# Kernel optimization log

Hardware: AMD Instinct MI355X
Metric: run time of the kernel (lower is better)

Reference implementation:

```python
import jax, jax.numpy as jnp
import numpy as np

B, C, H, W = 2, 64, 96, 96
HEADS, POOL, RED = 4, 2, 16
DH = C // HEADS  # dim_head = 16


def _conv1x1(x, Wt, b):
    # 1x1 conv == channelwise linear: Wt [Cout, Cin], x [B,Cin,H,W]
    return jnp.einsum('oc,bchw->bohw', Wt, x) + b[None, :, None, None]


def setup_inputs() -> dict:
    key = jax.random.key(0)
    ks = jax.random.split(key, 16)
    def w(k, shape, fan):
        return (jax.random.normal(k, shape, jnp.float32) / np.sqrt(fan)).astype(jnp.float32)
    x = jax.random.normal(ks[0], (B, C, H, W), jnp.float32)
    return {
        'x': x,
        'Wq': w(ks[1], (C, C), C), 'bq': jnp.zeros((C,), jnp.float32),
        'Wk': w(ks[2], (C, C), C), 'bk': jnp.zeros((C,), jnp.float32),
        'Wv': w(ks[3], (C, C), C), 'bv': jnp.zeros((C,), jnp.float32),
        'Wo': w(ks[4], (C, C), C), 'bo': jnp.zeros((C,), jnp.float32),
        'W1': w(ks[5], (C // RED, C), C), 'b1': jnp.zeros((C // RED,), jnp.float32),
        'W2': w(ks[6], (C, C // RED), C // RED), 'b2': jnp.zeros((C,), jnp.float32),
        'Wg': w(ks[7], (C, 2 * C), 2 * C), 'bg': jnp.zeros((C,), jnp.float32),
    }


def reference(x, Wq, bq, Wk, bk, Wv, bv, Wo, bo, W1, b1, W2, b2, Wg, bg):
    b, c, h, wdt = x.shape
    # --- MHSA with KV avg-pool downsampling (use_zoom=False -> zoomed_x = x) ---
    q = _conv1x1(x, Wq, bq)
    k = _conv1x1(x, Wk, bk)
    v = _conv1x1(x, Wv, bv)
    kh_, kw_ = h // POOL, wdt // POOL
    k = k.reshape(b, c, kh_, POOL, kw_, POOL).mean(axis=(3, 5))  # AvgPool2d(POOL)
    v = v.reshape(b, c, kh_, POOL, kw_, POOL).mean(axis=(3, 5))
    # reshape to heads: [B, heads, N, dh]
    qh = q.reshape(b, HEADS, DH, h * wdt).transpose(0, 1, 3, 2)
    kh = k.reshape(b, HEADS, DH, kh_ * kw_).transpose(0, 1, 3, 2)
    vh = v.reshape(b, HEADS, DH, kh_ * kw_).transpose(0, 1, 3, 2)
    scale = 1.0 / np.sqrt(DH)
    attn = jax.nn.softmax(jnp.einsum('bhqd,bhkd->bhqk', qh, kh) * scale, axis=-1)
    out = jnp.einsum('bhqk,bhkd->bhqd', attn, vh)  # [B,heads,N,dh]
    out = out.transpose(0, 1, 3, 2).reshape(b, c, h, wdt)
    attn_out = _conv1x1(out, Wo, bo)
    # --- SE excitation ---
    gap = attn_out.mean(axis=(2, 3))                      # [B,C]
    se = jax.nn.relu(gap @ W1.T + b1)                     # [B,C/r]
    ca = jax.nn.sigmoid(se @ W2.T + b2)                   # [B,C]
    enhanced = attn_out * ca[:, :, None, None]
    # --- residual fusion (use_zoom=False path) ---
    fused = x + enhanced
    # --- learned gate: concat GAPs -> 1x1 conv -> sigmoid -> blend ---
    gi = jnp.concatenate([x.mean(axis=(2, 3)), fused.mean(axis=(2, 3))], axis=1)  # [B,2C]
    gate = jax.nn.sigmoid(gi @ Wg.T + bg)[:, :, None, None]                       # [B,C,1,1]
    return x * (1.0 - gate) + fused * gate
```

## Files before the change

### kernel.cpp

```cpp
#include <hip/hip_runtime.h>
#include <hip/hip_bf16.h>

#define NPIX 9216
#define MKEY 2304

typedef __bf16 bf16x8 __attribute__((ext_vector_type(8)));
typedef float f32x4 __attribute__((ext_vector_type(4)));
typedef float f32x16 __attribute__((ext_vector_type(16)));
typedef short short8v __attribute__((ext_vector_type(8)));
typedef unsigned int u32x4v __attribute__((ext_vector_type(4)));

static __device__ __forceinline__ short f2bs(float f) {
  __bf16 h = (__bf16)f;
  return __builtin_bit_cast(short, h);
}

static __device__ __forceinline__ short4 pack4(const f32x16& acc, int q0, float4 bv, float scl) {
  short4 s;
  s.x = f2bs((acc[q0 + 0] + bv.x) * scl);
  s.y = f2bs((acc[q0 + 1] + bv.y) * scl);
  s.z = f2bs((acc[q0 + 2] + bv.z) * scl);
  s.w = f2bs((acc[q0 + 3] + bv.w) * scl);
  return s;
}

static __device__ __forceinline__ bf16x8 ldf8(const float* p) {
  float4 a = *(const float4*)p;
  float4 b = *(const float4*)(p + 4);
  bf16x8 f;
  f[0] = (__bf16)a.x; f[1] = (__bf16)a.y; f[2] = (__bf16)a.z; f[3] = (__bf16)a.w;
  f[4] = (__bf16)b.x; f[5] = (__bf16)b.y; f[6] = (__bf16)b.z; f[7] = (__bf16)b.w;
  return f;
}

__global__ __launch_bounds__(256) void proj_kernel(const float* __restrict__ x,
                                                   const float* __restrict__ Wq,
                                                   const float* __restrict__ bq,
                                                   const float* __restrict__ Wk,
                                                   const float* __restrict__ bk,
                                                   const float* __restrict__ Wv,
                                                   const float* __restrict__ bv,
                                                   short* __restrict__ qout,
                                                   short* __restrict__ kout,
                                                   short* __restrict__ vout,
                                                   short* __restrict__ onesb,
                                                   float* __restrict__ mxpart) {
  __shared__ float xs[64 * 128];
  int jid = blockIdx.x;
  int t = threadIdx.x;
  int w = t >> 6, lane = t & 63;
  int c31 = lane & 31, h5 = lane >> 5;
  bool isQ = jid < 144;
  int b, n0;
  if (isQ) { b = jid / 72; n0 = (jid % 72) * 128; }
  else { int j2 = jid - 144; b = j2 / 18; n0 = (j2 % 18) * 128; }

  if (jid == 0 && t < 160) {
    short8v ov;
#pragma unroll
    for (int j = 0; j < 8; j++) ov[j] = (short)0x3F80;
    *(short8v*)(onesb + t * 8) = ov;
  }

  if (isQ) {
#pragma unroll
    for (int i = 0; i < 8; i++) {
      int idx4 = t + 256 * i;
      int ci = idx4 >> 5, px4 = idx4 & 31;
      float4 v = *(const float4*)(x + ((size_t)(b * 64 + ci)) * NPIX + n0 + px4 * 4);
      *(float4*)(xs + ci * 128 + px4 * 4) = v;
    }
  } else {
#pragma unroll
    for (int it = 0; it < 32; it++) {
      int idx = t + 256 * it;
      int ci = idx >> 7, pm = idx & 127;
      int m = n0 + pm;
      int i = m / 48, j = m - i * 48;
      const float* s = x + ((size_t)(b * 64 + ci)) * NPIX + (2 * i) * 96 + 2 * j;
      float2 a = *(const float2*)(s);
      float2 c = *(const float2*)(s + 96);
      xs[ci * 128 + pm] = 0.25f * (a.x + a.y + c.x + c.y);
    }
  }
  __syncthreads();

  int px = w * 32 + c31;
  bf16x8 xf[4];
#pragma unroll
  for (int ks = 0; ks < 4; ks++) {
    bf16x8 f;
#pragma unroll
    for (int j = 0; j < 8; j++) f[j] = (__bf16)xs[(ks * 16 + h5 * 8 + j) * 128 + px];
    xf[ks] = f;
  }

  if (isQ) {
    int ci = t >> 2, qq = t & 3;
    const float* row = xs + ci * 128 + qq * 32;
    float s = 0.f;
#pragma unroll
    for (int i = 0; i < 32; i++) s += row[i];
    s += __shfl_xor(s, 1, 64);
    s += __shfl_xor(s, 2, 64);
    if (qq == 0) mxpart[jid * 64 + ci] = s;
  }
  __syncthreads();

  short* sv = (short*)xs;
  const float QSCALE = 0.25f * 1.44269504088896f;
  int nsets = isQ ? 1 : 2;

  for (int set = 0; set < nsets; set++) {
    const float* W = isQ ? Wq : (set ? Wv : Wk);
    const float* bias = isQ ? bq : (set ? bv : bk);
#pragma unroll
    for (int oc = 0; oc < 2; oc++) {
      bf16x8 wf[4];
#pragma unroll
      for (int ks = 0; ks < 4; ks++)
        wf[ks] = ldf8(W + (size_t)(oc * 32 + c31) * 64 + ks * 16 + h5 * 8);
      f32x16 acc = {};
#pragma unroll
      for (int ks = 0; ks < 4; ks++)
        acc = __builtin_amdgcn_mfma_f32_32x32x16_bf16(wf[ks], xf[ks], acc, 0, 0, 0);

      const float* bb = bias + oc * 32 + 4 * h5;
      float4 bv0 = *(const float4*)(bb);
      float4 bv1 = *(const float4*)(bb + 8);
      float4 bv2 = *(const float4*)(bb + 16);
      float4 bv3 = *(const float4*)(bb + 24);

      if (isQ || set == 0) {
        short* outp = isQ ? qout : kout;
        size_t NP = isQ ? NPIX : MKEY;
        float scl = isQ ? QSCALE : 1.0f;
        short* p0 = outp + (((size_t)(b * 4 + oc * 2)) * NP + n0 + px) * 16;
        short* p1 = outp + (((size_t)(b * 4 + oc * 2 + 1)) * NP + n0 + px) * 16;
        *(short4*)(p0 + 4 * h5) = pack4(acc, 0, bv0, scl);
        *(short4*)(p0 + 8 + 4 * h5) = pack4(acc, 4, bv1, scl);
        *(short4*)(p1 + 4 * h5) = pack4(acc, 8, bv2, scl);
        *(short4*)(p1 + 8 + 4 * h5) = pack4(acc, 12, bv3, scl);
      } else {
        float4 bvs[4] = {bv0, bv1, bv2, bv3};
#pragma unroll
        for (int g = 0; g < 4; g++) {
          int rowb = oc * 32 + 8 * g + 4 * h5;
          const float4& bv = bvs[g];
          sv[(rowb + 0) * 128 + px] = f2bs(acc[g * 4 + 0] + bv.x);
          sv[(rowb + 1) * 128 + px] = f2bs(acc[g * 4 + 1] + bv.y);
          sv[(rowb + 2) * 128 + px] = f2bs(acc[g * 4 + 2] + bv.z);
          sv[(rowb + 3) * 128 + px] = f2bs(acc[g * 4 + 3] + bv.w);
        }
      }
    }
  }

  if (!isQ) {
    __syncthreads();
#pragma unroll
    for (int kx = 0; kx < 4; kx++) {
      int idx8 = t + 256 * kx;
      int co = idx8 >> 4, pm8 = idx8 & 15;
      short8v v = *(short8v*)(sv + co * 128 + pm8 * 8);
      *(short8v*)(vout + ((size_t)(b * 64 + co)) * MKEY + n0 + pm8 * 8) = v;
    }
  }
}

__global__ __launch_bounds__(256, 3) void attn_kernel(const short* __restrict__ qb,
                                                      const short* __restrict__ kb,
                                                      const short* __restrict__ vb,
                                                      const short* __restrict__ onesb,
                                                      short* __restrict__ aob,
                                                      float* __restrict__ papart) {
  __shared__ __align__(16) float xch[3][3][64 * 12];
  int tid = threadIdx.x;
  int w = tid >> 6, lane = tid & 63;
  int c31 = lane & 31, h5 = lane >> 5;
  int h = blockIdx.y, b = blockIdx.z;
  int bh = b * 4 + h;
  int q0 = blockIdx.x * 96;

  bf16x8 qf[3];
#pragma unroll
  for (int qt = 0; qt < 3; qt++)
    qf[qt] = *(const bf16x8*)(qb + ((size_t)bh * NPIX + q0 + qt * 32 + c31) * 16 + h5 * 8);

  const short* kBh = kb + ((size_t)bh * MKEY + w * 576) * 16;
  const short* vsrc = (c31 < 16)
      ? (vb + ((size_t)(b * 64 + h * 16 + c31)) * MKEY + w * 576)
      : onesb;

  f32x16 zf16 = {};
  f32x16 oacc[3] = {zf16, zf16, zf16};

  bf16x8 nka0 = *(const bf16x8*)(kBh + (size_t)(c31) * 16 + h5 * 8);
  bf16x8 nka1 = *(const bf16x8*)(kBh + (size_t)(32 + c31) * 16 + h5 * 8);
  bf16x8 nva0 = *(const bf16x8*)(vsrc + h5 * 8);
  bf16x8 nva1 = *(const bf16x8*)(vsrc + 16 + h5 * 8);
  bf16x8 nva2 = *(const bf16x8*)(vsrc + 32 + h5 * 8);
  bf16x8 nva3 = *(const bf16x8*)(vsrc + 48 + h5 * 8);

  for (int kt = 0; kt < 9; kt++) {
    bf16x8 ka0 = nka0, ka1 = nka1;
    bf16x8 va0 = nva0, va1 = nva1, va2 = nva2, va3 = nva3;
    if (kt < 8) {
      int nb = (kt + 1) * 64;
      nka0 = *(const bf16x8*)(kBh + (size_t)(nb + c31) * 16 + h5 * 8);
      nka1 = *(const bf16x8*)(kBh + (size_t)(nb + 32 + c31) * 16 + h5 * 8);
      nva0 = *(const bf16x8*)(vsrc + nb + h5 * 8);
      nva1 = *(const bf16x8*)(vsrc + nb + 16 + h5 * 8);
      nva2 = *(const bf16x8*)(vsrc + nb + 32 + h5 * 8);
      nva3 = *(const bf16x8*)(vsrc + nb + 48 + h5 * 8);
    }

#pragma unroll
    for (int qt = 0; qt < 3; qt++) {
      f32x16 s0 = __builtin_amdgcn_mfma_f32_32x32x16_bf16(ka0, qf[qt], zf16, 0, 0, 0);
      f32x16 s1 = __builtin_amdgcn_mfma_f32_32x32x16_bf16(ka1, qf[qt], zf16, 0, 0, 0);

      unsigned W[16];
#pragma unroll
      for (int t2 = 0; t2 < 2; t2++) {
        const f32x16& ss = t2 ? s1 : s0;
#pragma unroll
        for (int i = 0; i < 8; i++) {
          float p0 = __builtin_amdgcn_exp2f(ss[2 * i]);
          float p1 = __builtin_amdgcn_exp2f(ss[2 * i + 1]);
          unsigned r;
          asm("v_cvt_pk_bf16_f32 %0, %1, %2" : "=v"(r) : "v"(p0), "v"(p1));
          W[t2 * 8 + i] = r;
        }
      }
#pragma unroll
      for (int g4 = 0; g4 < 4; g4++) {
        asm("v_permlane32_swap_b32 %0, %1" : "+v"(W[4 * g4 + 0]), "+v"(W[4 * g4 + 2]));
        asm("v_permlane32_swap_b32 %0, %1" : "+v"(W[4 * g4 + 1]), "+v"(W[4 * g4 + 3]));
      }
      u32x4v w0 = {W[0], W[1], W[2], W[3]};
      u32x4v w1 = {W[4], W[5], W[6], W[7]};
      u32x4v w2 = {W[8], W[9], W[10], W[11]};
      u32x4v w3 = {W[12], W[13], W[14], W[15]};
      oacc[qt] = __builtin_amdgcn_mfma_f32_32x32x16_bf16(va0, __builtin_bit_cast(bf16x8, w0), oacc[qt], 0, 0, 0);
      oacc[qt] = __builtin_amdgcn_mfma_f32_32x32x16_bf16(va1, __builtin_bit_cast(bf16x8, w1), oacc[qt], 0, 0, 0);
      oacc[qt] = __builtin_amdgcn_mfma_f32_32x32x16_bf16(va2, __builtin_bit_cast(bf16x8, w2), oacc[qt], 0, 0, 0);
      oacc[qt] = __builtin_amdgcn_mfma_f32_32x32x16_bf16(va3, __builtin_bit_cast(bf16x8, w3), oacc[qt], 0, 0, 0);
    }
  }

  if (w > 0) {
#pragma unroll
    for (int qt = 0; qt < 3; qt++) {
      float* p = xch[w - 1][qt] + lane * 12;
      p[0] = oacc[qt][8];
      f32x4 oa = {oacc[qt][0], oacc[qt][1], oacc[qt][2], oacc[qt][3]};
      f32x4 ob = {oacc[qt][4], oacc[qt][5], oacc[qt][6], oacc[qt][7]};
      *(f32x4*)(p + 4) = oa;
      *(f32x4*)(p + 8) = ob;
    }
  }
  __syncthreads();
  if (w == 0) {
    float psum[8];
#pragma unroll
    for (int k = 0; k < 8; k++) psum[k] = 0.f;
#pragma unroll
    for (int qt = 0; qt < 3; qt++) {
      const float* p1 = xch[0][qt] + lane * 12;
      const float* p2 = xch[1][qt] + lane * 12;
      const float* p3 = xch[2][qt] + lane * 12;
      float L = oacc[qt][8] + p1[0] + p2[0] + p3[0];
      float rinv = 1.0f / L;
      f32x4 o1a = *(const f32x4*)(p1 + 4), o1b = *(const f32x4*)(p1 + 8);
      f32x4 o2a = *(const f32x4*)(p2 + 4), o2b = *(const f32x4*)(p2 + 8);
      f32x4 o3a = *(const f32x4*)(p3 + 4), o3b = *(const f32x4*)(p3 + 8);
      float r0[4], r1[4];
#pragma unroll
      for (int j = 0; j < 4; j++) {
        r0[j] = (oacc[qt][j] + o1a[j] + o2a[j] + o3a[j]) * rinv;
        r1[j] = (oacc[qt][4 + j] + o1b[j] + o2b[j] + o3b[j]) * rinv;
        psum[j] += r0[j];
        psum[4 + j] += r1[j];
      }
      short* aop = aob + ((size_t)bh * NPIX + q0 + qt * 32 + c31) * 16;
      short4 t0, t1;
      t0.x = f2bs(r0[0]); t0.y = f2bs(r0[1]); t0.z = f2bs(r0[2]); t0.w = f2bs(r0[3]);
      t1.x = f2bs(r1[0]); t1.y = f2bs(r1[1]); t1.z = f2bs(r1[2]); t1.w = f2bs(r1[3]);
      *(short4*)(aop + h5 * 4) = t0;
      *(short4*)(aop + 8 + h5 * 4) = t1;
    }
#pragma unroll
    for (int mask = 1; mask <= 16; mask <<= 1)
#pragma unroll
      for (int k = 0; k < 8; k++) psum[k] += __shfl_xor(psum[k], mask, 64);
    if (c31 == 0) {
      float* pp = papart + ((size_t)blockIdx.x * 8 + bh) * 16;
      f32x4 pa = {psum[0], psum[1], psum[2], psum[3]};
      f32x4 pb = {psum[4], psum[5], psum[6], psum[7]};
      *(f32x4*)(pp + h5 * 4) = pa;
      *(f32x4*)(pp + 8 + h5 * 4) = pb;
    }
  }
}

__global__ __launch_bounds__(256) void se_gate_kernel(const float* __restrict__ mxpart,
                                                      const float* __restrict__ papart,
                                                      const float* __restrict__ Wo,
                                                      const float* __restrict__ bo,
                                                      const float* __restrict__ W1,
                                                      const float* __restrict__ b1,
                                                      const float* __restrict__ W2,
                                                      const float* __restrict__ b2,
                                                      const float* __restrict__ Wg,
                                                      const float* __restrict__ bg,
                                                      float* __restrict__ gfac) {
  __shared__ float ma_s[128], gap_s[128], ca_s[128], mx_s[128];
  __shared__ float ma2[128], mx2[128];
  int t = threadIdx.x;
  int tc = t & 127;
  int half = t >> 7;
  int b = tc >> 6, c = tc & 63;
  int hh = c >> 4, d = c & 15;
  float sa = 0.f;
  for (int bx = half * 48; bx < half * 48 + 48; bx++)
    sa += papart[((size_t)bx * 8 + b * 4 + hh) * 16 + d];
  float sx = 0.f;
  for (int j = half * 36; j < half * 36 + 36; j++)
    sx += mxpart[(b * 72 + j) * 64 + c];
  if (half == 0) { ma_s[tc] = sa; mx_s[tc] = sx; }
  else { ma2[tc] = sa; mx2[tc] = sx; }
  __syncthreads();
  if (t < 128) {
    ma_s[t] = (ma_s[t] + ma2[t]) * (1.f / NPIX);
    mx_s[t] = (mx_s[t] + mx2[t]) * (1.f / NPIX);
  }
  __syncthreads();
  if (t < 128) {
    float gp = bo[c];
    for (int ci = 0; ci < 64; ci++) gp += Wo[c * 64 + ci] * ma_s[b * 64 + ci];
    gap_s[t] = gp;
  }
  __syncthreads();
  if (t < 128) {
    float se[4];
#pragma unroll
    for (int i = 0; i < 4; i++) {
      float s = b1[i];
      for (int cc = 0; cc < 64; cc++) s += W1[i * 64 + cc] * gap_s[b * 64 + cc];
      se[i] = fmaxf(s, 0.f);
    }
    float cav = b2[c];
#pragma unroll
    for (int i = 0; i < 4; i++) cav += W2[c * 4 + i] * se[i];
    cav = 1.f / (1.f + __expf(-cav));
    ca_s[t] = cav;
  }
  __syncthreads();
  if (t < 128) {
    float gv = bg[c];
    for (int j = 0; j < 64; j++) gv += Wg[c * 128 + j] * mx_s[b * 64 + j];
    for (int j = 0; j < 64; j++)
      gv += Wg[c * 128 + 64 + j] * (mx_s[b * 64 + j] + ca_s[b * 64 + j] * gap_s[b * 64 + j]);
    gv = 1.f / (1.f + __expf(-gv));
    gfac[t] = gv * ca_s[t];
  }
}

__global__ __launch_bounds__(64) void oproj_final_kernel(const short* __restrict__ aob,
                                                         const float* __restrict__ W,
                                                         const float* __restrict__ bias,
                                                         const float* __restrict__ x,
                                                         const float* __restrict__ gfac,
                                                         float* __restrict__ out) {
  int b = blockIdx.y;
  int n0 = blockIdx.x * 32;
  int lane = threadIdx.x;
  int c31 = lane & 31, h5 = lane >> 5;
  int px = n0 + c31;

  bf16x8 xf[4];
#pragma unroll
  for (int ks = 0; ks < 4; ks++)
    xf[ks] = *(const bf16x8*)(aob + (((size_t)(b * 4 + ks)) * NPIX + px) * 16 + h5 * 8);

#pragma unroll
  for (int oc = 0; oc < 2; oc++) {
    bf16x8 wf[4];
#pragma unroll
    for (int ks = 0; ks < 4; ks++)
      wf[ks] = ldf8(W + (size_t)(oc * 32 + c31) * 64 + ks * 16 + h5 * 8);
    f32x16 acc = {};
#pragma unroll
    for (int ks = 0; ks < 4; ks++)
      acc = __builtin_amdgcn_mfma_f32_32x32x16_bf16(wf[ks], xf[ks], acc, 0, 0, 0);

    const float* bb = bias + oc * 32 + 4 * h5;
    const float* gg = gfac + b * 64 + oc * 32 + 4 * h5;
#pragma unroll
    for (int grp = 0; grp < 4; grp++) {
      float4 bv = *(const float4*)(bb + 8 * grp);
      float4 gf = *(const float4*)(gg + 8 * grp);
      int co = oc * 32 + 8 * grp + 4 * h5;
      const float* xp = x + ((size_t)(b * 64 + co)) * NPIX + px;
      float* op = out + ((size_t)(b * 64 + co)) * NPIX + px;
      op[0 * NPIX] = xp[0 * NPIX] + gf.x * (acc[grp * 4 + 0] + bv.x);
      op[1 * NPIX] = xp[1 * NPIX] + gf.y * (acc[grp * 4 + 1] + bv.y);
      op[2 * NPIX] = xp[2 * NPIX] + gf.z * (acc[grp * 4 + 2] + bv.z);
      op[3 * NPIX] = xp[3 * NPIX] + gf.w * (acc[grp * 4 + 3] + bv.w);
    }
  }
}

extern "C" void kernel_launch(void* const* d_in, const int* in_sizes, int n_in,
                              void* d_out, int out_size, void* d_ws, size_t ws_size,
                              hipStream_t stream) {
  const float* x  = (const float*)d_in[0];
  const float* Wq = (const float*)d_in[1];
  const float* bq = (const float*)d_in[2];
  const float* Wk = (const float*)d_in[3];
  const float* bk = (const float*)d_in[4];
  const float* Wv = (const float*)d_in[5];
  const float* bv = (const float*)d_in[6];
  const float* Wo = (const float*)d_in[7];
  const float* bo = (const float*)d_in[8];
  const float* W1 = (const float*)d_in[9];
  const float* b1 = (const float*)d_in[10];
  const float* W2 = (const float*)d_in[11];
  const float* b2 = (const float*)d_in[12];
  const float* Wg = (const float*)d_in[13];
  const float* bg = (const float*)d_in[14];

  char* w = (char*)d_ws;
  short* qb16   = (short*)w; w += 2359296;
  short* kb16   = (short*)w; w += 589824;
  short* vb16   = (short*)w; w += 589824;
  short* aob    = (short*)w; w += 2359296;
  float* mxpart = (float*)w; w += 36864;
  float* papart = (float*)w; w += 49152;
  float* gfac   = (float*)w; w += 512;
  short* onesb  = (short*)w; w += 2560;

  proj_kernel<<<180, 256, 0, stream>>>(x, Wq, bq, Wk, bk, Wv, bv, qb16, kb16, vb16, onesb, mxpart);
  attn_kernel<<<dim3(96, 4, 2), 256, 0, stream>>>(qb16, kb16, vb16, onesb, aob, papart);
  se_gate_kernel<<<1, 256, 0, stream>>>(mxpart, papart, Wo, bo, W1, b1, W2, b2, Wg, bg, gfac);
  oproj_final_kernel<<<dim3(288, 2), 64, 0, stream>>>(aob, Wo, bo, x, gfac, (float*)d_out);
}
```

Baseline: 56.01 us.

## Halve projection tile size to double block count and interleave softmax/PV MFMAs

The projection kernel now uses 64-pixel tiles, launching 360 blocks instead of 180. In the Q blocks each wave computes one output-channel half, and in the K/V blocks each wave handles one (set, oc) pair across two pixel groups, which spreads work over more CUs on a short, latency-bound kernel. The mxpart partial sums double in count, and the SE/gate reduction and workspace sizes are updated to match. In the attention kernel, the exp/convert/permlane/PV-MFMA work for the first 32-key half now runs before the second QK MFMA is issued, which reduces live registers and lets the two halves interleave.

```diff
diff --git a/kernel.cpp b/kernel.cpp
--- a/kernel.cpp
+++ b/kernel.cpp
@@ -45,15 +45,13 @@
                                                    short* __restrict__ vout,
                                                    short* __restrict__ onesb,
                                                    float* __restrict__ mxpart) {
-  __shared__ float xs[64 * 128];
+  __shared__ float xs[64 * 64];
   int jid = blockIdx.x;
   int t = threadIdx.x;
   int w = t >> 6, lane = t & 63;
   int c31 = lane & 31, h5 = lane >> 5;
-  bool isQ = jid < 144;
-  int b, n0;
-  if (isQ) { b = jid / 72; n0 = (jid % 72) * 128; }
-  else { int j2 = jid - 144; b = j2 / 18; n0 = (j2 % 18) * 128; }
+  bool isQ = jid < 288;
+  const float QSCALE = 0.25f * 1.44269504088896f;
 
   if (jid == 0 && t < 160) {
     short8v ov;
@@ -63,107 +61,137 @@
   }
 
   if (isQ) {
-#pragma unroll
-    for (int i = 0; i < 8; i++) {
+    int b = jid / 144, n0 = (jid % 144) * 64;
+#pragma unroll
+    for (int i = 0; i < 4; i++) {
       int idx4 = t + 256 * i;
-      int ci = idx4 >> 5, px4 = idx4 & 31;
+      int ci = idx4 >> 4, px4 = idx4 & 15;
       float4 v = *(const float4*)(x + ((size_t)(b * 64 + ci)) * NPIX + n0 + px4 * 4);
-      *(float4*)(xs + ci * 128 + px4 * 4) = v;
-    }
+      *(float4*)(xs + ci * 64 + px4 * 4) = v;
+    }
+    __syncthreads();
+
+    int px = (w >> 1) * 32 + c31;
+    int oc = w & 1;
+    bf16x8 xf[4];
+#pragma unroll
+    for (int ks = 0; ks < 4; ks++) {
+      bf16x8 f;
+#pragma unroll
+      for (int j = 0; j < 8; j++) f[j] = (__bf16)xs[(ks * 16 + h5 * 8 + j) * 64 + px];
+      xf[ks] = f;
+    }
+
+    {
+      int ci = t >> 2, qq = t & 3;
+      const float* row = xs + ci * 64 + qq * 16;
+      float s = 0.f;
+#pragma unroll
+      for (int i = 0; i < 16; i++) s += row[i];
+      s += __shfl_xor(s, 1, 64);
+      s += __shfl_xor(s, 2, 64);
+      if (qq == 0) mxpart[jid * 64 + ci] = s;
+    }
+
+    bf16x8 wf[4];
+#pragma unroll
+    for (int ks = 0; ks < 4; ks++)
+      wf[ks] = ldf8(Wq + (size_t)(oc * 32 + c31) * 64 + ks * 16 + h5 * 8);
+    f32x16 acc = {};
+#pragma unroll
+    for (int ks = 0; ks < 4; ks++)
+      acc = __builtin_amdgcn_mfma_f32_32x32x16_bf16(wf[ks], xf[ks], acc, 0, 0, 0);
+
+    const float* bb = bq + oc * 32 + 4 * h5;
+    float4 bv0 = *(const float4*)(bb);
+    float4 bv1 = *(const float4*)(bb + 8);
+    float4 bv2 = *(const float4*)(bb + 16);
+    float4 bv3 = *(const float4*)(bb + 24);
+    short* p0 = qout + (((size_t)(b * 4 + oc * 2)) * NPIX + n0 + px) * 16;
+    short* p1 = qout + (((size_t)(b * 4 + oc * 2 + 1)) * NPIX + n0 + px) * 16;
+    *(short4*)(p0 + 4 * h5) = pack4(acc, 0, bv0, QSCALE);
+    *(short4*)(p0 + 8 + 4 * h5) = pack4(acc, 4, bv1, QSCALE);
+    *(short4*)(p1 + 4 * h5) = pack4(acc, 8, bv2, QSCALE);
+    *(short4*)(p1 + 8 + 4 * h5) = pack4(acc, 12, bv3, QSCALE);
   } else {
-#pragma unroll
-    for (int it = 0; it < 32; it++) {
+    int j2 = jid - 288;
+    int b = j2 / 36, m0 = (j2 % 36) * 64;
+#pragma unroll
+    for (int it = 0; it < 16; it++) {
       int idx = t + 256 * it;
-      int ci = idx >> 7, pm = idx & 127;
-      int m = n0 + pm;
+      int ci = idx >> 6, pm = idx & 63;
+      int m = m0 + pm;
       int i = m / 48, j = m - i * 48;
       const float* s = x + ((size_t)(b * 64 + ci)) * NPIX + (2 * i) * 96 + 2 * j;
       float2 a = *(const float2*)(s);
       float2 c = *(const float2*)(s + 96);
-      xs[ci * 128 + pm] = 0.25f * (a.x + a.y + c.x + c.y);
-    }
-  }
-  __syncthreads();
-
-  int px = w * 32 + c31;
-  bf16x8 xf[4];
-#pragma unroll
-  for (int ks = 0; ks < 4; ks++) {
-    bf16x8 f;
-#pragma unroll
-    for (int j = 0; j < 8; j++) f[j] = (__bf16)xs[(ks * 16 + h5 * 8 + j) * 128 + px];
-    xf[ks] = f;
-  }
-
-  if (isQ) {
-    int ci = t >> 2, qq = t & 3;
-    const float* row = xs + ci * 128 + qq * 32;
-    float s = 0.f;
-#pragma unroll
-    for (int i = 0; i < 32; i++) s += row[i];
-    s += __shfl_xor(s, 1, 64);
-    s += __shfl_xor(s, 2, 64);
-    if (qq == 0) mxpart[jid * 64 + ci] = s;
-  }
-  __syncthreads();
-
-  short* sv = (short*)xs;
-  const float QSCALE = 0.25f * 1.44269504088896f;
-  int nsets = isQ ? 1 : 2;
-
-  for (int set = 0; set < nsets; set++) {
-    const float* W = isQ ? Wq : (set ? Wv : Wk);
-    const float* bias = isQ ? bq : (set ? bv : bk);
-#pragma unroll
-    for (int oc = 0; oc < 2; oc++) {
-      bf16x8 wf[4];
+      xs[ci * 64 + pm] = 0.25f * (a.x + a.y + c.x + c.y);
+    }
+    __syncthreads();
+
+    int set = w >> 1, oc = w & 1;
+    const float* W = set ? Wv : Wk;
+    const float* bias = set ? bv : bk;
+
+    bf16x8 xf[2][4];
+#pragma unroll
+    for (int mg = 0; mg < 2; mg++) {
+      int px = mg * 32 + c31;
+#pragma unroll
+      for (int ks = 0; ks < 4; ks++) {
+        bf16x8 f;
+#pragma unroll
+        for (int j = 0; j < 8; j++) f[j] = (__bf16)xs[(ks * 16 + h5 * 8 + j) * 64 + px];
+        xf[mg][ks] = f;
+      }
+    }
+    bf16x8 wf[4];
+#pragma unroll
+    for (int ks = 0; ks < 4; ks++)
+      wf[ks] = ldf8(W + (size_t)(oc * 32 + c31) * 64 + ks * 16 + h5 * 8);
+    const float* bb = bias + oc * 32 + 4 * h5;
+    float4 bv0 = *(const float4*)(bb);
+    float4 bv1 = *(const float4*)(bb + 8);
+    float4 bv2 = *(const float4*)(bb + 16);
+    float4 bv3 = *(const float4*)(bb + 24);
+    __syncthreads();
+
+    short* sv = (short*)xs;
+#pragma unroll
+    for (int mg = 0; mg < 2; mg++) {
+      int px = mg * 32 + c31;
+      f32x16 acc = {};
 #pragma unroll
       for (int ks = 0; ks < 4; ks++)
-        wf[ks] = ldf8(W + (size_t)(oc * 32 + c31) * 64 + ks * 16 + h5 * 8);
-      f32x16 acc = {};
-#pragma unroll
-      for (int ks = 0; ks < 4; ks++)
-        acc = __builtin_amdgcn_mfma_f32_32x32x16_bf16(wf[ks], xf[ks], acc, 0, 0, 0);
-
-      const float* bb = bias + oc * 32 + 4 * h5;
-      float4 bv0 = *(const float4*)(bb);
-      float4 bv1 = *(const float4*)(bb + 8);
-      float4 bv2 = *(const float4*)(bb + 16);
-      float4 bv3 = *(const float4*)(bb + 24);
-
-      if (isQ || set == 0) {
-        short* outp = isQ ? qout : kout;
-        size_t NP = isQ ? NPIX : MKEY;
-        float scl = isQ ? QSCALE : 1.0f;
-        short* p0 = outp + (((size_t)(b * 4 + oc * 2)) * NP + n0 + px) * 16;
-        short* p1 = outp + (((size_t)(b * 4 + oc * 2 + 1)) * NP + n0 + px) * 16;
-        *(short4*)(p0 + 4 * h5) = pack4(acc, 0, bv0, scl);
-        *(short4*)(p0 + 8 + 4 * h5) = pack4(acc, 4, bv1, scl);
-        *(short4*)(p1 + 4 * h5) = pack4(acc, 8, bv2, scl);
-        *(short4*)(p1 + 8 + 4 * h5) = pack4(acc, 12, bv3, scl);
+        acc = __builtin_amdgcn_mfma_f32_32x32x16_bf16(wf[ks], xf[mg][ks], acc, 0, 0, 0);
+
+      if (set == 0) {
+        short* p0 = kout + (((size_t)(b * 4 + oc * 2)) * MKEY + m0 + px) * 16;
+        short* p1 = kout + (((size_t)(b * 4 + oc * 2 + 1)) * MKEY + m0 + px) * 16;
+        *(short4*)(p0 + 4 * h5) = pack4(acc, 0, bv0, 1.0f);
+        *(short4*)(p0 + 8 + 4 * h5) = pack4(acc, 4, bv1, 1.0f);
+        *(short4*)(p1 + 4 * h5) = pack4(acc, 8, bv2, 1.0f);
+        *(short4*)(p1 + 8 + 4 * h5) = pack4(acc, 12, bv3, 1.0f);
       } else {
         float4 bvs[4] = {bv0, bv1, bv2, bv3};
 #pragma unroll
         for (int g = 0; g < 4; g++) {
           int rowb = oc * 32 + 8 * g + 4 * h5;
           const float4& bv = bvs[g];
-          sv[(rowb + 0) * 128 + px] = f2bs(acc[g * 4 + 0] + bv.x);
-          sv[(rowb + 1) * 128 + px] = f2bs(acc[g * 4 + 1] + bv.y);
-          sv[(rowb + 2) * 128 + px] = f2bs(acc[g * 4 + 2] + bv.z);
-          sv[(rowb + 3) * 128 + px] = f2bs(acc[g * 4 + 3] + bv.w);
+          sv[(rowb + 0) * 64 + px] = f2bs(acc[g * 4 + 0] + bv.x);
+          sv[(rowb + 1) * 64 + px] = f2bs(acc[g * 4 + 1] + bv.y);
+          sv[(rowb + 2) * 64 + px] = f2bs(acc[g * 4 + 2] + bv.z);
+          sv[(rowb + 3) * 64 + px] = f2bs(acc[g * 4 + 3] + bv.w);
         }
       }
     }
-  }
-
-  if (!isQ) {
     __syncthreads();
 #pragma unroll
-    for (int kx = 0; kx < 4; kx++) {
+    for (int kx = 0; kx < 2; kx++) {
       int idx8 = t + 256 * kx;
-      int co = idx8 >> 4, pm8 = idx8 & 15;
-      short8v v = *(short8v*)(sv + co * 128 + pm8 * 8);
-      *(short8v*)(vout + ((size_t)(b * 64 + co)) * MKEY + n0 + pm8 * 8) = v;
+      int co = idx8 >> 3, pm8 = idx8 & 7;
+      short8v v = *(short8v*)(sv + co * 64 + pm8 * 8);
+      *(short8v*)(vout + ((size_t)(b * 64 + co)) * MKEY + m0 + pm8 * 8) = v;
     }
   }
 }
@@ -218,34 +246,45 @@
 #pragma unroll
     for (int qt = 0; qt < 3; qt++) {
       f32x16 s0 = __builtin_amdgcn_mfma_f32_32x32x16_bf16(ka0, qf[qt], zf16, 0, 0, 0);
-      f32x16 s1 = __builtin_amdgcn_mfma_f32_32x32x16_bf16(ka1, qf[qt], zf16, 0, 0, 0);
-
-      unsigned W[16];
-#pragma unroll
-      for (int t2 = 0; t2 < 2; t2++) {
-        const f32x16& ss = t2 ? s1 : s0;
+      {
+        unsigned W[8];
 #pragma unroll
         for (int i = 0; i < 8; i++) {
-          float p0 = __builtin_amdgcn_exp2f(ss[2 * i]);
-          float p1 = __builtin_amdgcn_exp2f(ss[2 * i + 1]);
+          float p0 = __builtin_amdgcn_exp2f(s0[2 * i]);
+          float p1 = __builtin_amdgcn_exp2f(s0[2 * i + 1]);
           unsigned r;
           asm("v_cvt_pk_bf16_f32 %0, %1, %2" : "=v"(r) : "v"(p0), "v"(p1));
-          W[t2 * 8 + i] = r;
+          W[i] = r;
         }
+        asm("v_permlane32_swap_b32 %0, %1" : "+v"(W[0]), "+v"(W[2]));
+        asm("v_permlane32_swap_b32 %0, %1" : "+v"(W[1]), "+v"(W[3]));
+        asm("v_permlane32_swap_b32 %0, %1" : "+v"(W[4]), "+v"(W[6]));
+        asm("v_permlane32_swap_b32 %0, %1" : "+v"(W[5]), "+v"(W[7]));
+        u32x4v w0 = {W[0], W[1], W[2], W[3]};
+        u32x4v w1 = {W[4], W[5], W[6], W[7]};
+        oacc[qt] = __builtin_amdgcn_mfma_f32_32x32x16_bf16(va0, __builtin_bit_cast(bf16x8, w0), oacc[qt], 0, 0, 0);
+        oacc[qt] = __builtin_amdgcn_mfma_f32_32x32x16_bf16(va1, __builtin_bit_cast(bf16x8, w1), oacc[qt], 0, 0, 0);
       }
-#pragma unroll
-      for (int g4 = 0; g4 < 4; g4++) {
-        asm("v_permlane32_swap_b32 %0, %1" : "+v"(W[4 * g4 + 0]), "+v"(W[4 * g4 + 2]));
-        asm("v_permlane32_swap_b32 %0, %1" : "+v"(W[4 * g4 + 1]), "+v"(W[4 * g4 + 3]));
+      f32x16 s1 = __builtin_amdgcn_mfma_f32_32x32x16_bf16(ka1, qf[qt], zf16, 0, 0, 0);
+      {
+        unsigned W[8];
+#pragma unroll
+        for (int i = 0; i < 8; i++) {
+          float p0 = __builtin_amdgcn_exp2f(s1[2 * i]);
+          float p1 = __builtin_amdgcn_exp2f(s1[2 * i + 1]);
+          unsigned r;
+          asm("v_cvt_pk_bf16_f32 %0, %1, %2" : "=v"(r) : "v"(p0), "v"(p1));
+          W[i] = r;
+        }
+        asm("v_permlane32_swap_b32 %0, %1" : "+v"(W[0]), "+v"(W[2]));
+        asm("v_permlane32_swap_b32 %0, %1" : "+v"(W[1]), "+v"(W[3]));
+        asm("v_permlane32_swap_b32 %0, %1" : "+v"(W[4]), "+v"(W[6]));
+        asm("v_permlane32_swap_b32 %0, %1" : "+v"(W[5]), "+v"(W[7]));
+        u32x4v w2 = {W[0], W[1], W[2], W[3]};
+        u32x4v w3 = {W[4], W[5], W[6], W[7]};
+        oacc[qt] = __builtin_amdgcn_mfma_f32_32x32x16_bf16(va2, __builtin_bit_cast(bf16x8, w2), oacc[qt], 0, 0, 0);
+        oacc[qt] = __builtin_amdgcn_mfma_f32_32x32x16_bf16(va3, __builtin_bit_cast(bf16x8, w3), oacc[qt], 0, 0, 0);
       }
-      u32x4v w0 = {W[0], W[1], W[2], W[3]};
-      u32x4v w1 = {W[4], W[5], W[6], W[7]};
-      u32x4v w2 = {W[8], W[9], W[10], W[11]};
-      u32x4v w3 = {W[12], W[13], W[14], W[15]};
-      oacc[qt] = __builtin_amdgcn_mfma_f32_32x32x16_bf16(va0, __builtin_bit_cast(bf16x8, w0), oacc[qt], 0, 0, 0);
-      oacc[qt] = __builtin_amdgcn_mfma_f32_32x32x16_bf16(va1, __builtin_bit_cast(bf16x8, w1), oacc[qt], 0, 0, 0);
-      oacc[qt] = __builtin_amdgcn_mfma_f32_32x32x16_bf16(va2, __builtin_bit_cast(bf16x8, w2), oacc[qt], 0, 0, 0);
-      oacc[qt] = __builtin_amdgcn_mfma_f32_32x32x16_bf16(va3, __builtin_bit_cast(bf16x8, w3), oacc[qt], 0, 0, 0);
     }
   }
 
@@ -326,8 +365,8 @@
   for (int bx = half * 48; bx < half * 48 + 48; bx++)
     sa += papart[((size_t)bx * 8 + b * 4 + hh) * 16 + d];
   float sx = 0.f;
-  for (int j = half * 36; j < half * 36 + 36; j++)
-    sx += mxpart[(b * 72 + j) * 64 + c];
+  for (int j = half * 72; j < half * 72 + 72; j++)
+    sx += mxpart[(b * 144 + j) * 64 + c];
   if (half == 0) { ma_s[tc] = sa; mx_s[tc] = sx; }
   else { ma2[tc] = sa; mx2[tc] = sx; }
   __syncthreads();
@@ -436,12 +475,12 @@
   short* kb16   = (short*)w; w += 589824;
   short* vb16   = (short*)w; w += 589824;
   short* aob    = (short*)w; w += 2359296;
-  float* mxpart = (float*)w; w += 36864;
+  float* mxpart = (float*)w; w += 73728;
   float* papart = (float*)w; w += 49152;
   float* gfac   = (float*)w; w += 512;
   short* onesb  = (short*)w; w += 2560;
 
-  proj_kernel<<<180, 256, 0, stream>>>(x, Wq, bq, Wk, bk, Wv, bv, qb16, kb16, vb16, onesb, mxpart);
+  proj_kernel<<<360, 256, 0, stream>>>(x, Wq, bq, Wk, bk, Wv, bv, qb16, kb16, vb16, onesb, mxpart);
   attn_kernel<<<dim3(96, 4, 2), 256, 0, stream>>>(qb16, kb16, vb16, onesb, aob, papart);
   se_gate_kernel<<<1, 256, 0, stream>>>(mxpart, papart, Wo, bo, W1, b1, W2, b2, Wg, bg, gfac);
   oproj_final_kernel<<<dim3(288, 2), 64, 0, stream>>>(aob, Wo, bo, x, gfac, (float*)d_out);
```

New measurement: 54.46 us (median of 3 runs). -2.8%, faster.
